# Optimization experiments

Hardware: AMD Instinct MI355X
Metric: run time of the kernel (lower is better)

Reference implementation:

```python
import jax, jax.numpy as jnp
import numpy as np
import math

B, S, D = 8, 1024, 1024
H = 4
QK_DIM = D // 8          # hyp qk_dim_div = 8
EXPAND_DIM = 2 * D       # hyp expand_factor = 2
V_DIM = D
RESIDUAL_DEPTH = 384     # hyp['net']['residual_depth'] for model_scale=1.0
NUM_BLOCKS = 8
LN_EPS = 1e-5


def setup_inputs() -> dict:
    key = jax.random.key(0)
    k1, k2, k3 = jax.random.split(key, 3)
    x = jax.random.normal(k1, (B, S, D), dtype=jnp.float32)
    attn_mask = jnp.tril(jnp.ones((S, S), dtype=bool))  # causal boolean mask
    norm_w = jnp.ones((D,), dtype=jnp.float32)
    expand_scale = 0.5 * (1.0 / RESIDUAL_DEPTH ** 0.5) * 0.5  # 1/expand_factor
    expand_w = expand_scale * jax.random.normal(k2, (2 * QK_DIM + 2 * EXPAND_DIM, D), dtype=jnp.float32)
    project_scale = (1.0 / RESIDUAL_DEPTH ** 0.5) * 0.5 * (1.0 / NUM_BLOCKS)
    project_w = project_scale * jax.random.normal(k3, (D, EXPAND_DIM), dtype=jnp.float32)
    position_bias_mult = jnp.asarray(1.0, dtype=jnp.float32)
    return {"x": x, "attn_mask": attn_mask, "norm_w": norm_w,
            "expand_w": expand_w, "project_w": project_w,
            "position_bias_mult": position_bias_mult}


def reference(x, attn_mask, norm_w, expand_w, project_w, position_bias_mult):
    b, s, d = x.shape
    residual = x
    # ALiBi-style additive bias: position_bias_base[i, j] = j - i (<= 0 on causal part)
    pos = jnp.arange(s)
    bias_base = (pos[None, :] - pos[:, None]).astype(x.dtype)
    bias = jnp.where(attn_mask,
                     jax.nn.softplus(position_bias_mult) * bias_base,
                     -jnp.inf)  # [s, s], broadcasts over (b, h)

    # LayerNorm (no bias)
    mu = jnp.mean(x, axis=-1, keepdims=True)
    var = jnp.mean(jnp.square(x - mu), axis=-1, keepdims=True)
    xn = (x - mu) * jax.lax.rsqrt(var + LN_EPS) * norm_w

    # fused expand: [q | k | linear | pre_gelu]
    h = jnp.einsum('bsd,ed->bse', xn, expand_w)
    q = h[..., :QK_DIM]
    k = h[..., QK_DIM:2 * QK_DIM]
    lin = h[..., 2 * QK_DIM:2 * QK_DIM + EXPAND_DIM]
    pre = h[..., 2 * QK_DIM + EXPAND_DIM:]
    geglu = lin * jax.nn.gelu(pre, approximate=False)  # torch F.gelu default = exact

    # linear_value = False: both local and attention value come from geglu
    geglu_local = geglu[..., :EXPAND_DIM - V_DIM]
    geglu_value = geglu[..., EXPAND_DIM - V_DIM:]

    def split_heads(t):  # b s (h d) -> b h s d
        return t.reshape(b, s, H, -1).transpose(0, 2, 1, 3)

    qh, kh, vh, gl = map(split_heads, (q, k, geglu_value, geglu_local))
    scale = 1.0 / math.sqrt(qh.shape[-1])
    scores = jnp.einsum('bhqd,bhkd->bhqk', qh, kh) * scale + bias
    attn = jax.nn.softmax(scores, axis=-1)
    att_out = jnp.einsum('bhqk,bhkd->bhqd', attn, vh)

    def merge_heads(t):  # b h s d -> b s (h d)
        return t.transpose(0, 2, 1, 3).reshape(b, s, -1)

    fused = jnp.concatenate([merge_heads(gl), merge_heads(att_out)], axis=-1)
    out = jnp.einsum('bse,de->bsd', fused, project_w)
    return residual + out
```

## Files before the change

kernel.cpp:

```cpp
#include <hip/hip_runtime.h>
#include <hip/hip_bf16.h>
#include <hip/hip_fp8.h>

typedef __bf16 bf16x8 __attribute__((ext_vector_type(8)));
typedef __bf16 bf16x4 __attribute__((ext_vector_type(4)));
typedef float f32x4 __attribute__((ext_vector_type(4)));
typedef unsigned int u32;
typedef __attribute__((address_space(3))) u32 lds_u32_t;
typedef __attribute__((address_space(1))) u32 glb_u32_t;

#define MROWS 8192
#define DDIM 1024
#define EDIM 2048
#define HQK 256

#define S_BAR() asm volatile("s_barrier" ::: "memory")
#define S_VM0() asm volatile("s_waitcnt vmcnt(0)" ::: "memory")
#define SCHED_PIN() __builtin_amdgcn_sched_barrier(0)

__device__ __forceinline__ void async16(const void* g, void* l) {
  __builtin_amdgcn_global_load_lds((const glb_u32_t*)g, (lds_u32_t*)l, 16, 0, 0);
}

__device__ __forceinline__ u32 pack4_e4m3(float f0, float f1, float f2, float f3) {
  __hip_fp8_e4m3 a(f0), b(f1), c(f2), d(f3);
  return (u32)a.__x | ((u32)b.__x << 8) | ((u32)c.__x << 16) | ((u32)d.__x << 24);
}

__global__ __launch_bounds__(256) void ln_kernel(const float* __restrict__ x,
                                                 const float* __restrict__ wgt,
                                                 __bf16* __restrict__ xn,
                                                 u32* __restrict__ xn8) {
  const int row = blockIdx.x;
  const int t = threadIdx.x;
  const float4 v = ((const float4*)(x + (size_t)row * DDIM))[t];
  float s = v.x + v.y + v.z + v.w;
  float ss = v.x * v.x + v.y * v.y + v.z * v.z + v.w * v.w;
  #pragma unroll
  for (int o = 32; o > 0; o >>= 1) {
    s += __shfl_down(s, o);
    ss += __shfl_down(ss, o);
  }
  __shared__ float red[8];
  const int lane = t & 63, wv = t >> 6;
  if (lane == 0) { red[wv] = s; red[4 + wv] = ss; }
  __syncthreads();
  s = red[0] + red[1] + red[2] + red[3];
  ss = red[4] + red[5] + red[6] + red[7];
  const float mu = s * (1.0f / 1024.0f);
  const float rstd = rsqrtf(ss * (1.0f / 1024.0f) - mu * mu + 1e-5f);
  const float4 w4 = ((const float4*)wgt)[t];
  const float f0 = (v.x - mu) * rstd * w4.x;
  const float f1 = (v.y - mu) * rstd * w4.y;
  const float f2 = (v.z - mu) * rstd * w4.z;
  const float f3 = (v.w - mu) * rstd * w4.w;
  bf16x4 o;
  o[0] = (__bf16)f0; o[1] = (__bf16)f1; o[2] = (__bf16)f2; o[3] = (__bf16)f3;
  ((bf16x4*)(xn + (size_t)row * DDIM))[t] = o;
  xn8[row * 256 + t] = pack4_e4m3(f0, f1, f2, f3);
}

__global__ __launch_bounds__(256) void cast_kernel(const float* __restrict__ src,
                                                   __bf16* __restrict__ dst, int n4) {
  const int i = blockIdx.x * 256 + threadIdx.x;
  if (i < n4) {
    const float4 v = ((const float4*)src)[i];
    bf16x4 o;
    o[0] = (__bf16)v.x; o[1] = (__bf16)v.y; o[2] = (__bf16)v.z; o[3] = (__bf16)v.w;
    ((bf16x4*)dst)[i] = o;
  }
}

__global__ __launch_bounds__(256) void cast8_kernel(const float* __restrict__ src,
                                                    u32* __restrict__ dst, int n4, float scale) {
  const int i = blockIdx.x * 256 + threadIdx.x;
  if (i < n4) {
    const float4 v = ((const float4*)src)[i];
    dst[i] = pack4_e4m3(v.x * scale, v.y * scale, v.z * scale, v.w * scale);
  }
}

__global__ __launch_bounds__(256) void cast8i_kernel(const float* __restrict__ src,
                                                     u32* __restrict__ dst) {
  const int i = blockIdx.x * 256 + threadIdx.x;
  const int rp = i >> 8, k4 = i & 255;
  const int c = ((rp >> 5) << 4) | (rp & 15);
  const int pre = (rp >> 4) & 1;
  const float4 v = *(const float4*)(src + ((size_t)(pre * 2048 + c)) * 1024 + k4 * 4);
  dst[i] = pack4_e4m3(v.x * 16.0f, v.y * 16.0f, v.z * 16.0f, v.w * 16.0f);
}

__global__ __launch_bounds__(256) void gemm_bt(const __bf16* __restrict__ A,
                                               const __bf16* __restrict__ Bt,
                                               __bf16* __restrict__ Cout,
                                               int Ndim, int Kdim, int coff) {
  __shared__ __bf16 As[128 * 32];
  __shared__ __bf16 Bs[128 * 32];
  const int t = threadIdx.x;
  const int lane = t & 63;
  const int w = t >> 6;
  const int wm = w >> 1, wn = w & 1;
  const int m0 = blockIdx.x * 128;
  const int n0 = blockIdx.y * 128;

  f32x4 acc[4][4] = {};

  const int cA = w * 2;
  const int sr = cA * 16 + (lane >> 2);
  const int sc = (lane & 3) * 8;
  const __bf16* gA0 = A + (size_t)(m0 + sr) * Kdim + sc;
  const __bf16* gA1 = A + (size_t)(m0 + sr + 16) * Kdim + sc;
  const __bf16* gB0 = Bt + (size_t)(n0 + sr) * Kdim + sc;
  const __bf16* gB1 = Bt + (size_t)(n0 + sr + 16) * Kdim + sc;
  __bf16* lA0 = As + cA * 512;
  __bf16* lA1 = As + (cA + 1) * 512;
  __bf16* lB0 = Bs + cA * 512;
  __bf16* lB1 = Bs + (cA + 1) * 512;

  const int lr = lane & 15;
  const int lk = (lane >> 4) * 8;
  const int nk = Kdim >> 5;

  for (int kt = 0; kt < nk; ++kt) {
    __syncthreads();
    const int ko = kt * 32;
    async16(gA0 + ko, lA0);
    async16(gA1 + ko, lA1);
    async16(gB0 + ko, lB0);
    async16(gB1 + ko, lB1);
    __syncthreads();
    bf16x8 a[4], b[4];
    #pragma unroll
    for (int i = 0; i < 4; ++i)
      a[i] = *(const bf16x8*)&As[(wm * 64 + i * 16 + lr) * 32 + lk];
    #pragma unroll
    for (int i = 0; i < 4; ++i)
      b[i] = *(const bf16x8*)&Bs[(wn * 64 + i * 16 + lr) * 32 + lk];
    #pragma unroll
    for (int i = 0; i < 4; ++i)
      #pragma unroll
      for (int j = 0; j < 4; ++j)
        acc[i][j] = __builtin_amdgcn_mfma_f32_16x16x32_bf16(a[i], b[j], acc[i][j], 0, 0, 0);
  }

  #pragma unroll
  for (int i = 0; i < 4; ++i) {
    const int rbase = m0 + wm * 64 + i * 16 + ((lane >> 4) << 2);
    #pragma unroll
    for (int j = 0; j < 4; ++j) {
      const int col = coff + n0 + wn * 64 + j * 16 + (lane & 15);
      #pragma unroll
      for (int r = 0; r < 4; ++r)
        Cout[(size_t)(rbase + r) * Ndim + col] = (__bf16)acc[i][j][r];
    }
  }
}

__global__ __launch_bounds__(512, 4) void gemm1glu(const char* __restrict__ A8,
                                                   const char* __restrict__ B8,
                                                   char* __restrict__ fused8,
                                                   char* __restrict__ vbuf8) {
  constexpr int ASZ = 128 * 64;
  constexpr int BSZ = 256 * 64;
  constexpr int Kdim = 1024;
  __shared__ alignas(16) char As[2 * ASZ];
  __shared__ alignas(16) char Bs[2 * BSZ];

  const int tid = threadIdx.x;
  const int lane = tid & 63;
  const int w = tid >> 6;
  const int wm = w >> 2, wn = w & 3;

  const int qq = gridDim.x >> 3;
  const int wgid = (blockIdx.x & 7) * qq + (blockIdx.x >> 3);
  const int m0 = (wgid / 16) * 128;
  const int nblk = wgid % 16;
  const int n0r = nblk * 256;

  f32x4 acc[4][4] = {};

  const int rowS = (tid >> 2) & 127;
  const int uS = tid & 3;
  const int luS = uS ^ ((rowS >> 1) & 3);
  const char* gA = A8 + (size_t)(m0 + rowS) * Kdim + luS * 16;
  const char* gB = B8 + (size_t)(n0r + rowS) * Kdim + luS * 16;
  char* lA = (char*)As;
  char* lB = (char*)Bs;

  const int lr = lane & 15;
  const int hi = lane >> 4;
  const int sw = (lr >> 1) & 3;
  const int kof0 = ((((hi >> 1)) ^ sw) << 4) + (hi & 1) * 8;
  const int kof1 = (((2 + (hi >> 1)) ^ sw) << 4) + (hi & 1) * 8;
  const int rowA = (wm * 64 + lr) * 64;
  const int rowB = (wn * 64 + lr) * 64;
  const int NT = Kdim >> 6;

  async16(gA, lA + tid * 16);
  async16(gB, lB + tid * 16);
  async16(gB + (size_t)128 * Kdim, lB + 8192 + tid * 16);
  S_VM0();
  S_BAR();

  for (int t = 0; t < NT; ++t) {
    const int buf = t & 1;
    const char* pA = lA + buf * ASZ + rowA;
    const char* pB = lB + buf * BSZ + rowB;

    long a0[4], b0[4], a1[4], b1[4];
    #pragma unroll
    for (int ni = 0; ni < 4; ++ni) b0[ni] = *(const long*)(pB + ni * 1024 + kof0);
    #pragma unroll
    for (int mi = 0; mi < 4; ++mi) a0[mi] = *(const long*)(pA + mi * 1024 + kof0);
    SCHED_PIN();
    #pragma unroll
    for (int ni = 0; ni < 4; ++ni) b1[ni] = *(const long*)(pB + ni * 1024 + kof1);
    #pragma unroll
    for (int mi = 0; mi < 4; ++mi) a1[mi] = *(const long*)(pA + mi * 1024 + kof1);
    SCHED_PIN();
    if (t + 1 < NT) {
      const char* gAt = gA + (size_t)(t + 1) * 64;
      const char* gBt = gB + (size_t)(t + 1) * 64;
      char* lAd = lA + (buf ^ 1) * ASZ + tid * 16;
      char* lBd = lB + (buf ^ 1) * BSZ + tid * 16;
      async16(gAt, lAd);
      async16(gBt, lBd);
      async16(gBt + (size_t)128 * Kdim, lBd + 8192);
    }
    SCHED_PIN();
    __builtin_amdgcn_s_setprio(1);
    #pragma unroll
    for (int mi = 0; mi < 4; ++mi)
      #pragma unroll
      for (int ni = 0; ni < 4; ++ni)
        acc[mi][ni] = __builtin_amdgcn_mfma_f32_16x16x32_fp8_fp8(a0[mi], b0[ni], acc[mi][ni], 0, 0, 0);
    __builtin_amdgcn_s_setprio(0);
    SCHED_PIN();
    __builtin_amdgcn_s_setprio(1);
    #pragma unroll
    for (int mi = 0; mi < 4; ++mi)
      #pragma unroll
      for (int ni = 0; ni < 4; ++ni)
        acc[mi][ni] = __builtin_amdgcn_mfma_f32_16x16x32_fp8_fp8(a1[mi], b1[ni], acc[mi][ni], 0, 0, 0);
    __builtin_amdgcn_s_setprio(0);
    SCHED_PIN();
    if (t + 1 < NT) S_VM0();
    S_BAR();
  }

  const int col = lane & 15;
  const int cbase = nblk * 128 + wn * 32;
  const bool isv = nblk >= 8;
  #pragma unroll
  for (int mi = 0; mi < 4; ++mi) {
    const int rbase = m0 + wm * 64 + mi * 16 + (hi << 2);
    #pragma unroll
    for (int p = 0; p < 2; ++p) {
      const int c = cbase + p * 16 + col;
      #pragma unroll
      for (int r = 0; r < 4; ++r) {
        const float l = acc[mi][2 * p][r] * 0.0625f;
        const float q = acc[mi][2 * p + 1][r] * 0.0625f;
        const float g = l * 0.5f * q * (1.0f + erff(q * 0.70710678118f));
        __hip_fp8_e4m3 f8(g);
        if (isv) vbuf8[(size_t)(rbase + r) * 1024 + (c - 1024)] = (char)f8.__x;
        else     fused8[(size_t)(rbase + r) * EDIM + c] = (char)f8.__x;
      }
    }
  }
}

__global__ __launch_bounds__(512, 2) void gemmproj(const char* __restrict__ A8,
                                                   const char* __restrict__ B8,
                                                   float* __restrict__ out,
                                                   const float* __restrict__ resid,
                                                   float scl) {
  constexpr int ASZ = 64 * 128;
  constexpr int BSZ = 256 * 128;
  constexpr int Kdim = 2048;
  __shared__ alignas(16) char As[2 * ASZ];
  __shared__ alignas(16) char Bs[2 * BSZ];

  const int tid = threadIdx.x;
  const int lane = tid & 63;
  const int w = tid >> 6;
  const int wm = w >> 2, wn = w & 3;

  const int qq = gridDim.x >> 3;
  const int wgid = (blockIdx.x & 7) * qq + (blockIdx.x >> 3);
  const int m0 = (wgid / 4) * 64;
  const int n0 = (wgid % 4) * 256;

  f32x4 acc[2][4] = {};

  const int rowS = tid >> 3;
  const int uS = tid & 7;
  const int luS = uS ^ (rowS & 7);
  const char* gA = A8 + (size_t)(m0 + rowS) * Kdim + luS * 16;
  const char* gB = B8 + (size_t)(n0 + rowS) * Kdim + luS * 16;
  char* lA = (char*)As;
  char* lB = (char*)Bs;

  const int lr = lane & 15;
  const int hi = lane >> 4;
  int kof[4];
  #pragma unroll
  for (int kq = 0; kq < 4; ++kq)
    kof[kq] = (((kq * 2 + (hi >> 1)) ^ (lr & 7)) << 4) + (hi & 1) * 8;
  const int rowA = (wm * 32 + lr) * 128;
  const int rowB = (wn * 64 + lr) * 128;
  const int NT = Kdim >> 7;

  async16(gA, lA + tid * 16);
  #pragma unroll
  for (int c = 0; c < 4; ++c) async16(gB + (size_t)c * 64 * Kdim, lB + c * 8192 + tid * 16);
  S_VM0();
  S_BAR();

  for (int t = 0; t < NT; ++t) {
    const int buf = t & 1;
    const char* pA = lA + buf * ASZ + rowA;
    const char* pB = lB + buf * BSZ + rowB;

    long a[4][2], bb[4][4];
    #pragma unroll
    for (int kq = 0; kq < 4; ++kq) {
      #pragma unroll
      for (int ni = 0; ni < 4; ++ni) bb[kq][ni] = *(const long*)(pB + ni * 2048 + kof[kq]);
      #pragma unroll
      for (int mi = 0; mi < 2; ++mi) a[kq][mi] = *(const long*)(pA + mi * 2048 + kof[kq]);
    }
    SCHED_PIN();
    if (t + 1 < NT) {
      const char* gAt = gA + (size_t)(t + 1) * 128;
      const char* gBt = gB + (size_t)(t + 1) * 128;
      char* lAd = lA + (buf ^ 1) * ASZ + tid * 16;
      char* lBd = lB + (buf ^ 1) * BSZ + tid * 16;
      async16(gAt, lAd);
      #pragma unroll
      for (int c = 0; c < 4; ++c) async16(gBt + (size_t)c * 64 * Kdim, lBd + c * 8192);
    }
    SCHED_PIN();
    #pragma unroll
    for (int kq = 0; kq < 4; ++kq) {
      __builtin_amdgcn_s_setprio(1);
      #pragma unroll
      for (int mi = 0; mi < 2; ++mi)
        #pragma unroll
        for (int ni = 0; ni < 4; ++ni)
          acc[mi][ni] = __builtin_amdgcn_mfma_f32_16x16x32_fp8_fp8(a[kq][mi], bb[kq][ni], acc[mi][ni], 0, 0, 0);
      __builtin_amdgcn_s_setprio(0);
      SCHED_PIN();
    }
    if (t + 1 < NT) S_VM0();
    S_BAR();
  }

  #pragma unroll
  for (int mi = 0; mi < 2; ++mi) {
    const int rbase = m0 + wm * 32 + mi * 16 + (hi << 2);
    #pragma unroll
    for (int ni = 0; ni < 4; ++ni) {
      const int col = n0 + wn * 64 + ni * 16 + (lane & 15);
      #pragma unroll
      for (int r = 0; r < 4; ++r) {
        const size_t off = (size_t)(rbase + r) * DDIM + col;
        out[off] = resid[off] + acc[mi][ni][r] * scl;
      }
    }
  }
}

__global__ __launch_bounds__(256) void vT8_kernel(const char* __restrict__ vbuf8,
                                                  char* __restrict__ vTb) {
  const int blk = blockIdx.x;
  const int sblk = blk & 15;
  const int head = (blk >> 4) & 3;
  const int b = blk >> 6;
  const int t = threadIdx.x;
  __shared__ u32 vt[64][66];

  const int s_l = t >> 2, q4 = t & 3;
  const uint4* src = (const uint4*)&vbuf8[(size_t)(b * 1024 + sblk * 64 + s_l) * 1024 +
                                          head * 256 + q4 * 64];
  #pragma unroll
  for (int c = 0; c < 4; ++c) {
    const uint4 ww = src[c];
    vt[s_l][q4 * 16 + c * 4 + 0] = ww.x;
    vt[s_l][q4 * 16 + c * 4 + 1] = ww.y;
    vt[s_l][q4 * 16 + c * 4 + 2] = ww.z;
    vt[s_l][q4 * 16 + c * 4 + 3] = ww.w;
  }
  __syncthreads();
  const int d = t;
  const int wsel = (d & 3) * 8;
  char* dst = vTb + (((size_t)(b * 4 + head) * 16 + sblk) * 256 + d) * 64;
  #pragma unroll
  for (int c = 0; c < 4; ++c) {
    u32 wo[4];
    #pragma unroll
    for (int k = 0; k < 4; ++k) {
      const int s0 = c * 16 + k * 4;
      const u32 r0 = vt[s0 + 0][d >> 2];
      const u32 r1 = vt[s0 + 1][d >> 2];
      const u32 r2 = vt[s0 + 2][d >> 2];
      const u32 r3 = vt[s0 + 3][d >> 2];
      wo[k] = ((r0 >> wsel) & 0xffu) | (((r1 >> wsel) & 0xffu) << 8) |
              (((r2 >> wsel) & 0xffu) << 16) | (((r3 >> wsel) & 0xffu) << 24);
    }
    *(uint4*)(dst + c * 16) = make_uint4(wo[0], wo[1], wo[2], wo[3]);
  }
}

__global__ __launch_bounds__(256, 2) void attn_mfma(const __bf16* __restrict__ h,
                                                    const char* __restrict__ vTb,
                                                    char* __restrict__ fused8,
                                                    const float* __restrict__ pbm) {
  const int blk = blockIdx.x;
  const int qblk = blk & 7;
  const int head = (blk >> 3) & 3;
  const int b = blk >> 5;
  const int tid = threadIdx.x;
  const int lane = tid & 63;
  const int w = tid >> 6;
  __shared__ char vt[256 * 176];
  __shared__ char pl[4][32 * 80];

  const float p = pbm[0];
  const float sp = (p > 20.0f) ? p : log1pf(expf(p));

  {
    const int m = qblk * 2;
    const char* base = vTb + ((size_t)(b * 4 + head) * 16) * 16384;
    #pragma unroll
    for (int it = 0; it < 11; ++it) {
      const int U = it * 256 + tid;
      const int d = U / 11;
      const int slot = U - d * 11;
      int sb, so;
      if (slot >= 10)      { sb = m; so = 0; }
      else if (slot < 2)   { sb = m - 1; so = 32 + slot * 16; }
      else if (slot < 6)   { sb = m; so = (slot - 2) * 16; }
      else                 { sb = m + 1; so = (slot - 6) * 16; }
      if (sb < 0) sb = 0;
      async16(base + ((size_t)sb * 256 + d) * 64 + so, vt + U * 16);
    }
  }

  const int col = lane & 15;
  const int hi = lane >> 4;
  const int qb = qblk * 128 + w * 32;
  const int kb = qb - 32;

  f32x4 sc[4][2] = {};
  bf16x8 afr[4], bfr[2];
  #pragma unroll
  for (int mf = 0; mf < 4; ++mf) {
    int key = kb + mf * 16 + col;
    if (key < 0) key = 0;
    afr[mf] = *(const bf16x8*)&h[(size_t)(b * 1024 + key) * HQK + 128 + head * 32 + hi * 8];
  }
  #pragma unroll
  for (int nf = 0; nf < 2; ++nf)
    bfr[nf] = *(const bf16x8*)&h[(size_t)(b * 1024 + qb + nf * 16 + col) * HQK + head * 32 + hi * 8];
  #pragma unroll
  for (int mf = 0; mf < 4; ++mf)
    #pragma unroll
    for (int nf = 0; nf < 2; ++nf)
      sc[mf][nf] = __builtin_amdgcn_mfma_f32_16x16x32_bf16(afr[mf], bfr[nf], sc[mf][nf], 0, 0, 0);

  #pragma unroll
  for (int nf = 0; nf < 2; ++nf) {
    #pragma unroll
    for (int mf = 0; mf < 4; ++mf)
      #pragma unroll
      for (int r = 0; r < 4; ++r) {
        const int delta = mf * 16 + hi * 4 + r - nf * 16 - col - 32;
        const int keyabs = kb + mf * 16 + hi * 4 + r;
        const bool valid = (delta <= 0) & (delta >= -31) & (keyabs >= 0);
        sc[mf][nf][r] = valid ? sc[mf][nf][r] * 0.1767766953f + sp * (float)delta : -1e30f;
      }
    float m = -1e30f;
    #pragma unroll
    for (int mf = 0; mf < 4; ++mf)
      #pragma unroll
      for (int r = 0; r < 4; ++r) m = fmaxf(m, sc[mf][nf][r]);
    m = fmaxf(m, __shfl_xor(m, 16));
    m = fmaxf(m, __shfl_xor(m, 32));
    float s = 0.0f;
    #pragma unroll
    for (int mf = 0; mf < 4; ++mf)
      #pragma unroll
      for (int r = 0; r < 4; ++r) {
        const float e = __expf(sc[mf][nf][r] - m);
        sc[mf][nf][r] = e;
        s += e;
      }
    s += __shfl_xor(s, 16);
    s += __shfl_xor(s, 32);
    const float inv = 1.0f / s;
    #pragma unroll
    for (int mf = 0; mf < 4; ++mf) {
      const u32 pk = pack4_e4m3(sc[mf][nf][0] * inv, sc[mf][nf][1] * inv,
                                sc[mf][nf][2] * inv, sc[mf][nf][3] * inv);
      *(u32*)&pl[w][(nf * 16 + col) * 80 + mf * 16 + hi * 4] = pk;
    }
  }

  __syncthreads();

  const char* ppl = pl[w];
  const int kloc = w * 32;
  f32x4 ao[16][2] = {};
  #pragma unroll
  for (int kf = 0; kf < 2; ++kf) {
    long bfrag[2];
    #pragma unroll
    for (int nf = 0; nf < 2; ++nf)
      bfrag[nf] = *(const long*)&ppl[(nf * 16 + col) * 80 + kf * 32 + hi * 8];
    #pragma unroll
    for (int mf = 0; mf < 16; ++mf) {
      const long af = *(const long*)&vt[(mf * 16 + col) * 176 + kloc + kf * 32 + hi * 8];
      #pragma unroll
      for (int nf = 0; nf < 2; ++nf)
        ao[mf][nf] = __builtin_amdgcn_mfma_f32_16x16x32_fp8_fp8(af, bfrag[nf], ao[mf][nf], 0, 0, 0);
    }
  }

  #pragma unroll
  for (int mf = 0; mf < 16; ++mf)
    #pragma unroll
    for (int nf = 0; nf < 2; ++nf) {
      const u32 pk = pack4_e4m3(ao[mf][nf][0], ao[mf][nf][1], ao[mf][nf][2], ao[mf][nf][3]);
      *(u32*)&fused8[(size_t)(b * 1024 + qb + nf * 16 + col) * EDIM + 1024 +
                     head * 256 + mf * 16 + hi * 4] = pk;
    }
}

extern "C" void kernel_launch(void* const* d_in, const int* in_sizes, int n_in,
                              void* d_out, int out_size, void* d_ws, size_t ws_size,
                              hipStream_t stream) {
  const float* x = (const float*)d_in[0];
  const float* norm_w = (const float*)d_in[2];
  const float* expand_w = (const float*)d_in[3];
  const float* project_w = (const float*)d_in[4];
  const float* pbm = (const float*)d_in[5];
  float* out = (float*)d_out;

  char* ws = (char*)d_ws;
  __bf16* xn    = (__bf16*)(ws);
  u32*    xn8   = (u32*)(ws + 16777216);
  __bf16* wqk   = (__bf16*)(ws + 25165824);
  char*   wexp8i= (char*)(ws + 25690112);
  char*   wproj8= (char*)(ws + 29884416);
  __bf16* h     = (__bf16*)(ws + 31981568);
  char*   fused8= (char*)(ws + 36175872);
  char*   vbuf8 = (char*)(ws + 52953088);
  char*   vTb   = (char*)(ws + 61341696);

  ln_kernel<<<MROWS, 256, 0, stream>>>(x, norm_w, xn, xn8);
  cast_kernel<<<256, 256, 0, stream>>>(expand_w, wqk, 65536);
  cast8i_kernel<<<4096, 256, 0, stream>>>(expand_w + 256 * DDIM, (u32*)wexp8i);
  cast8_kernel<<<2048, 256, 0, stream>>>(project_w, (u32*)wproj8, 524288, 256.0f);
  gemm_bt<<<dim3(64, 2), 256, 0, stream>>>(xn, wqk, h, HQK, DDIM, 0);
  gemm1glu<<<1024, 512, 0, stream>>>((const char*)xn8, wexp8i, fused8, vbuf8);
  vT8_kernel<<<512, 256, 0, stream>>>(vbuf8, vTb);
  attn_mfma<<<256, 256, 0, stream>>>(h, vTb, fused8, pbm);
  gemmproj<<<512, 512, 0, stream>>>(fused8, wproj8, out, x, 1.0f / 256.0f);
}
```

Before: 152.2 us.

## Transpose expand MFMA for packed fp8 stores and retile projection GEMM to 128x128

In the expand GEMM the MFMA operands are swapped so each lane holds four consecutive output columns. The GEGLU epilogue can then pack four fp8 values and write them as one 32-bit store instead of four byte stores. The projection GEMM moves from 64x256 to 128x128 tiles, which changes the A/B load balance and the per-wave fragment shape and gives more balanced reuse. The grid size has to match the new tiling (wgid/8 rows), which relies on the host launching the same block count.

```diff
diff --git a/kernel.cpp b/kernel.cpp
--- a/kernel.cpp
+++ b/kernel.cpp
@@ -230,42 +230,41 @@
     SCHED_PIN();
     __builtin_amdgcn_s_setprio(1);
     #pragma unroll
-    for (int mi = 0; mi < 4; ++mi)
-      #pragma unroll
-      for (int ni = 0; ni < 4; ++ni)
-        acc[mi][ni] = __builtin_amdgcn_mfma_f32_16x16x32_fp8_fp8(a0[mi], b0[ni], acc[mi][ni], 0, 0, 0);
+    for (int ni = 0; ni < 4; ++ni)
+      #pragma unroll
+      for (int mi = 0; mi < 4; ++mi)
+        acc[ni][mi] = __builtin_amdgcn_mfma_f32_16x16x32_fp8_fp8(b0[ni], a0[mi], acc[ni][mi], 0, 0, 0);
     __builtin_amdgcn_s_setprio(0);
     SCHED_PIN();
     __builtin_amdgcn_s_setprio(1);
     #pragma unroll
-    for (int mi = 0; mi < 4; ++mi)
-      #pragma unroll
-      for (int ni = 0; ni < 4; ++ni)
-        acc[mi][ni] = __builtin_amdgcn_mfma_f32_16x16x32_fp8_fp8(a1[mi], b1[ni], acc[mi][ni], 0, 0, 0);
+    for (int ni = 0; ni < 4; ++ni)
+      #pragma unroll
+      for (int mi = 0; mi < 4; ++mi)
+        acc[ni][mi] = __builtin_amdgcn_mfma_f32_16x16x32_fp8_fp8(b1[ni], a1[mi], acc[ni][mi], 0, 0, 0);
     __builtin_amdgcn_s_setprio(0);
     SCHED_PIN();
     if (t + 1 < NT) S_VM0();
     S_BAR();
   }
 
-  const int col = lane & 15;
-  const int cbase = nblk * 128 + wn * 32;
   const bool isv = nblk >= 8;
   #pragma unroll
-  for (int mi = 0; mi < 4; ++mi) {
-    const int rbase = m0 + wm * 64 + mi * 16 + (hi << 2);
-    #pragma unroll
-    for (int p = 0; p < 2; ++p) {
-      const int c = cbase + p * 16 + col;
+  for (int p = 0; p < 2; ++p) {
+    const int cb = (nblk * 8 + wn * 2 + p) * 16 + hi * 4;
+    #pragma unroll
+    for (int mf = 0; mf < 4; ++mf) {
+      const int m = m0 + wm * 64 + mf * 16 + (lane & 15);
+      float g[4];
       #pragma unroll
       for (int r = 0; r < 4; ++r) {
-        const float l = acc[mi][2 * p][r] * 0.0625f;
-        const float q = acc[mi][2 * p + 1][r] * 0.0625f;
-        const float g = l * 0.5f * q * (1.0f + erff(q * 0.70710678118f));
-        __hip_fp8_e4m3 f8(g);
-        if (isv) vbuf8[(size_t)(rbase + r) * 1024 + (c - 1024)] = (char)f8.__x;
-        else     fused8[(size_t)(rbase + r) * EDIM + c] = (char)f8.__x;
+        const float l = acc[2 * p][mf][r] * 0.0625f;
+        const float q = acc[2 * p + 1][mf][r] * 0.0625f;
+        g[r] = l * 0.5f * q * (1.0f + erff(q * 0.70710678118f));
       }
+      const u32 pk = pack4_e4m3(g[0], g[1], g[2], g[3]);
+      if (isv) *(u32*)&vbuf8[(size_t)m * 1024 + (cb - 1024)] = pk;
+      else     *(u32*)&fused8[(size_t)m * EDIM + cb] = pk;
     }
   }
 }
@@ -275,8 +274,8 @@
                                                    float* __restrict__ out,
                                                    const float* __restrict__ resid,
                                                    float scl) {
-  constexpr int ASZ = 64 * 128;
-  constexpr int BSZ = 256 * 128;
+  constexpr int ASZ = 128 * 128;
+  constexpr int BSZ = 128 * 128;
   constexpr int Kdim = 2048;
   __shared__ alignas(16) char As[2 * ASZ];
   __shared__ alignas(16) char Bs[2 * BSZ];
@@ -288,10 +287,10 @@
 
   const int qq = gridDim.x >> 3;
   const int wgid = (blockIdx.x & 7) * qq + (blockIdx.x >> 3);
-  const int m0 = (wgid / 4) * 64;
-  const int n0 = (wgid % 4) * 256;
-
-  f32x4 acc[2][4] = {};
+  const int m0 = (wgid / 8) * 128;
+  const int n0 = (wgid % 8) * 128;
+
+  f32x4 acc[4][2] = {};
 
   const int rowS = tid >> 3;
   const int uS = tid & 7;
@@ -307,13 +306,14 @@
   #pragma unroll
   for (int kq = 0; kq < 4; ++kq)
     kof[kq] = (((kq * 2 + (hi >> 1)) ^ (lr & 7)) << 4) + (hi & 1) * 8;
-  const int rowA = (wm * 32 + lr) * 128;
-  const int rowB = (wn * 64 + lr) * 128;
+  const int rowA = (wm * 64 + lr) * 128;
+  const int rowB = (wn * 32 + lr) * 128;
   const int NT = Kdim >> 7;
 
   async16(gA, lA + tid * 16);
-  #pragma unroll
-  for (int c = 0; c < 4; ++c) async16(gB + (size_t)c * 64 * Kdim, lB + c * 8192 + tid * 16);
+  async16(gA + (size_t)64 * Kdim, lA + 8192 + tid * 16);
+  async16(gB, lB + tid * 16);
+  async16(gB + (size_t)64 * Kdim, lB + 8192 + tid * 16);
   S_VM0();
   S_BAR();
 
@@ -322,13 +322,13 @@
     const char* pA = lA + buf * ASZ + rowA;
     const char* pB = lB + buf * BSZ + rowB;
 
-    long a[4][2], bb[4][4];
+    long a[4][4], bb[4][2];
     #pragma unroll
     for (int kq = 0; kq < 4; ++kq) {
       #pragma unroll
-      for (int ni = 0; ni < 4; ++ni) bb[kq][ni] = *(const long*)(pB + ni * 2048 + kof[kq]);
-      #pragma unroll
-      for (int mi = 0; mi < 2; ++mi) a[kq][mi] = *(const long*)(pA + mi * 2048 + kof[kq]);
+      for (int ni = 0; ni < 2; ++ni) bb[kq][ni] = *(const long*)(pB + ni * 2048 + kof[kq]);
+      #pragma unroll
+      for (int mi = 0; mi < 4; ++mi) a[kq][mi] = *(const long*)(pA + mi * 2048 + kof[kq]);
     }
     SCHED_PIN();
     if (t + 1 < NT) {
@@ -337,17 +337,18 @@
       char* lAd = lA + (buf ^ 1) * ASZ + tid * 16;
       char* lBd = lB + (buf ^ 1) * BSZ + tid * 16;
       async16(gAt, lAd);
-      #pragma unroll
-      for (int c = 0; c < 4; ++c) async16(gBt + (size_t)c * 64 * Kdim, lBd + c * 8192);
+      async16(gAt + (size_t)64 * Kdim, lAd + 8192);
+      async16(gBt, lBd);
+      async16(gBt + (size_t)64 * Kdim, lBd + 8192);
     }
     SCHED_PIN();
     #pragma unroll
     for (int kq = 0; kq < 4; ++kq) {
       __builtin_amdgcn_s_setprio(1);
       #pragma unroll
-      for (int mi = 0; mi < 2; ++mi)
+      for (int mi = 0; mi < 4; ++mi)
         #pragma unroll
-        for (int ni = 0; ni < 4; ++ni)
+        for (int ni = 0; ni < 2; ++ni)
           acc[mi][ni] = __builtin_amdgcn_mfma_f32_16x16x32_fp8_fp8(a[kq][mi], bb[kq][ni], acc[mi][ni], 0, 0, 0);
       __builtin_amdgcn_s_setprio(0);
       SCHED_PIN();
@@ -357,11 +358,11 @@
   }
 
   #pragma unroll
-  for (int mi = 0; mi < 2; ++mi) {
-    const int rbase = m0 + wm * 32 + mi * 16 + (hi << 2);
-    #pragma unroll
-    for (int ni = 0; ni < 4; ++ni) {
-      const int col = n0 + wn * 64 + ni * 16 + (lane & 15);
+  for (int mi = 0; mi < 4; ++mi) {
+    const int rbase = m0 + wm * 64 + mi * 16 + (hi << 2);
+    #pragma unroll
+    for (int ni = 0; ni < 2; ++ni) {
+      const int col = n0 + wn * 32 + ni * 16 + (lane & 15);
       #pragma unroll
       for (int r = 0; r < 4; ++r) {
         const size_t off = (size_t)(rbase + r) * DDIM + col;
```

After: 152.5 us. About the same (+0.2%).
